# Optimization experiments

Measured on AMD Instinct MI355X. Metric: run time of the kernel, lower is better.

## Reference

```python
import jax, jax.numpy as jnp
import numpy as np

N = 20000      # nodes
E = 160000     # edges (avg degree 16)
IN_DIM = 256
HID = 128      # hidden_dim == per-head out_channels in PyG TransformerConv
HEADS = 4
EPS = 1e-5


def setup_inputs() -> dict:
    key = jax.random.key(0)
    ks = jax.random.split(key, 24)

    def w(k, shape, scale=0.05):
        return jax.random.normal(k, shape, dtype=jnp.float32) * scale

    inp = {
        "x": jax.random.normal(ks[0], (N, IN_DIM), dtype=jnp.float32),
        "edge_index": jax.random.randint(ks[1], (2, E), 0, N, dtype=jnp.int32),
        # input projection
        "lin_w": w(ks[2], (IN_DIM, HID)), "lin_b": jnp.zeros((HID,), jnp.float32),
    }
    i = 3
    for l in (1, 2):
        inp[f"q_w{l}"] = w(ks[i], (HID, HEADS * HID)); i += 1
        inp[f"q_b{l}"] = jnp.zeros((HEADS * HID,), jnp.float32)
        inp[f"k_w{l}"] = w(ks[i], (HID, HEADS * HID)); i += 1
        inp[f"k_b{l}"] = jnp.zeros((HEADS * HID,), jnp.float32)
        inp[f"v_w{l}"] = w(ks[i], (HID, HEADS * HID)); i += 1
        inp[f"v_b{l}"] = jnp.zeros((HEADS * HID,), jnp.float32)
        inp[f"s_w{l}"] = w(ks[i], (HID, HID)); i += 1
        inp[f"s_b{l}"] = jnp.zeros((HID,), jnp.float32)
        inp[f"ln_g{l}"] = jnp.ones((HID,), jnp.float32)
        inp[f"ln_b{l}"] = jnp.zeros((HID,), jnp.float32)
    return inp


def _segment_softmax(scores, seg, num):
    # scores: [E, HEADS], seg: [E] destination indices
    m = jax.ops.segment_max(scores, seg, num_segments=num)
    m = jnp.where(jnp.isfinite(m), m, 0.0)  # guard empty segments
    e = jnp.exp(scores - m[seg])
    d = jax.ops.segment_sum(e, seg, num_segments=num)
    return e / (d[seg] + 1e-16)


def _transformer_conv(x, src, dst, qw, qb, kw, kb, vw, vb, sw, sb):
    # PyG TransformerConv(HID, HID, heads=HEADS, concat=False)
    n = x.shape[0]
    q = (x @ qw + qb).reshape(n, HEADS, HID)
    k = (x @ kw + kb).reshape(n, HEADS, HID)
    v = (x @ vw + vb).reshape(n, HEADS, HID)
    # per-edge attention: query at dst (i), key/value at src (j)
    alpha = jnp.einsum("ehd,ehd->eh", q[dst], k[src]) / jnp.sqrt(jnp.float32(HID))
    alpha = _segment_softmax(alpha, dst, n)                 # [E, HEADS]
    msg = v[src] * alpha[..., None]                          # [E, HEADS, HID]
    out = jax.ops.segment_sum(msg, dst, num_segments=n)      # [N, HEADS, HID]
    out = out.mean(axis=1)                                   # concat=False -> head mean
    return out + x @ sw + sb                                 # root skip connection


def _layer_norm(x, g, b):
    mu = x.mean(-1, keepdims=True)
    var = ((x - mu) ** 2).mean(-1, keepdims=True)
    return (x - mu) * jax.lax.rsqrt(var + EPS) * g + b


def reference(x, edge_index, lin_w, lin_b,
              q_w1, q_b1, k_w1, k_b1, v_w1, v_b1, s_w1, s_b1, ln_g1, ln_b1,
              q_w2, q_b2, k_w2, k_b2, v_w2, v_b2, s_w2, s_b2, ln_g2, ln_b2):
    src, dst = edge_index[0], edge_index[1]
    h = jax.nn.relu(x @ lin_w + lin_b)
    h1 = _transformer_conv(h, src, dst, q_w1, q_b1, k_w1, k_b1, v_w1, v_b1, s_w1, s_b1)
    h = _layer_norm(h1 + h, ln_g1, ln_b1)
    h2 = _transformer_conv(h, src, dst, q_w2, q_b2, k_w2, k_b2, v_w2, v_b2, s_w2, s_b2)
    h = _layer_norm(h2 + h, ln_g2, ln_b2)
    return h
```

## Files before the change

### kernel.cpp

```cpp
#include <hip/hip_runtime.h>
#include <math.h>

#define NNODE 20000
#define NEDGE 160000
#define IN_DIMV 256
#define HIDV 128
#define DEGCAP 64

typedef __attribute__((ext_vector_type(8))) short bf16x8;
typedef __attribute__((ext_vector_type(4))) float f32x4;
typedef __attribute__((ext_vector_type(2))) float f32x2;

__device__ __forceinline__ float bf2f(unsigned short u) {
    union { unsigned int i; float f; } x; x.i = ((unsigned int)u) << 16; return x.f;
}
__device__ __forceinline__ unsigned short f2bf(float f) {
    union { float f; unsigned int i; } x; x.f = f;
    unsigned int r = x.i + 0x7fffu + ((x.i >> 16) & 1u);
    return (unsigned short)(r >> 16);
}
__device__ __forceinline__ void unpack8(uint4 p, float* f) {
    f[0] = bf2f((unsigned short)(p.x & 0xffff)); f[1] = bf2f((unsigned short)(p.x >> 16));
    f[2] = bf2f((unsigned short)(p.y & 0xffff)); f[3] = bf2f((unsigned short)(p.y >> 16));
    f[4] = bf2f((unsigned short)(p.z & 0xffff)); f[5] = bf2f((unsigned short)(p.z >> 16));
    f[6] = bf2f((unsigned short)(p.w & 0xffff)); f[7] = bf2f((unsigned short)(p.w >> 16));
}
__device__ __forceinline__ void unpack8f8_w(unsigned int a, unsigned int b, float* f) {
    f32x2 t;
    t = __builtin_amdgcn_cvt_pk_f32_fp8((int)a, false); f[0] = t.x; f[1] = t.y;
    t = __builtin_amdgcn_cvt_pk_f32_fp8((int)a, true);  f[2] = t.x; f[3] = t.y;
    t = __builtin_amdgcn_cvt_pk_f32_fp8((int)b, false); f[4] = t.x; f[5] = t.y;
    t = __builtin_amdgcn_cvt_pk_f32_fp8((int)b, true);  f[6] = t.x; f[7] = t.y;
}
__device__ __forceinline__ void unpack16f8(uint4 p, float* f) {
    unpack8f8_w(p.x, p.y, f);
    unpack8f8_w(p.z, p.w, f + 8);
}
__device__ __forceinline__ unsigned char f2fp8(float v) {
    int pk = __builtin_amdgcn_cvt_pk_fp8_f32(v, v, 0, false);
    return (unsigned char)(pk & 0xff);
}
__device__ __forceinline__ void gld_lds16(const unsigned short* g, unsigned short* l) {
    __builtin_amdgcn_global_load_lds((const __attribute__((address_space(1))) void*)g,
                                     (__attribute__((address_space(3))) void*)l, 16, 0, 0);
}

__global__ void convert_kernel(
    const float* __restrict__ x, const float* __restrict__ lin_w,
    const float* __restrict__ qw0, const float* __restrict__ kw0,
    const float* __restrict__ vw0, const float* __restrict__ sw0,
    const float* __restrict__ qw1, const float* __restrict__ kw1,
    const float* __restrict__ vw1, const float* __restrict__ sw1,
    unsigned short* __restrict__ xbf, unsigned short* __restrict__ arena)
{
    int idx = blockIdx.x * 256 + threadIdx.x;
    if (idx < 5120000) { xbf[idx] = f2bf(x[idx]); return; }
    int id2 = idx - 5120000;
    if (id2 >= 458752) return;
    float v;
    if (id2 < 32768) {
        int n = id2 >> 8, k = id2 & 255;
        v = lin_w[k * 128 + n];
    } else {
        int t = id2 - 32768;
        int l = t / 212992, r = t % 212992;
        int n = r >> 7, k = r & 127;
        const float* qw = l ? qw1 : qw0;
        const float* kw = l ? kw1 : kw0;
        const float* vw = l ? vw1 : vw0;
        const float* sw = l ? sw1 : sw0;
        if (n < 1536) {
            const float* w = (n < 512) ? qw : (n < 1024) ? kw : vw;
            v = w[k * 512 + (n & 511)];
        } else {
            v = sw[k * 128 + (n - 1536)];
        }
    }
    arena[id2] = f2bf(v);
}

template <int MODE, int K>
__global__ __launch_bounds__(256) void mfma_gemm(
    const unsigned short* __restrict__ A, const unsigned short* __restrict__ WT,
    const float* __restrict__ b0, const float* __restrict__ b1,
    const float* __restrict__ b2, const float* __restrict__ b3,
    unsigned short* __restrict__ qb_out, unsigned char* __restrict__ kv8_out,
    unsigned short* __restrict__ pre16_out, unsigned short* __restrict__ hbf_out)
{
    constexpr bool FULLK = (K == 128);
    __shared__ unsigned short smem[FULLK ? 32768 : 8192];
    unsigned short* ot = smem;
    unsigned char* ot8 = (unsigned char*)smem;

    int tid = threadIdx.x;
    int lane = tid & 63;
    int w = tid >> 6;
    int wm = w & 1, wn = w >> 1;
    int bm = blockIdx.x * 128;
    int bn = blockIdx.y * 128;

    int srow = lane >> 2;
    int scol = (lane & 3) * 8;
    int ar0 = bm + w * 32 + srow;      if (ar0 > NNODE - 1) ar0 = NNODE - 1;
    int ar1 = bm + w * 32 + 16 + srow; if (ar1 > NNODE - 1) ar1 = NNODE - 1;
    int br0 = bn + w * 32 + srow;
    int br1 = bn + w * 32 + 16 + srow;

    f32x4 acc[4][4] = {};
    int arow = wm * 64 + (lane & 15);
    int brow = wn * 64 + (lane & 15);
    int koff = (lane >> 4) * 8;

    if constexpr (FULLK) {
        unsigned short* As = smem;
        unsigned short* Bs = smem + 16384;
#pragma unroll
        for (int c = 0; c < 4; c++) {
            int k0 = c * 32;
            gld_lds16(A + (size_t)ar0 * K + k0 + scol, As + c * 4096 + (w * 32) * 32);
            gld_lds16(A + (size_t)ar1 * K + k0 + scol, As + c * 4096 + (w * 32 + 16) * 32);
            gld_lds16(WT + (size_t)br0 * K + k0 + scol, Bs + c * 4096 + (w * 32) * 32);
            gld_lds16(WT + (size_t)br1 * K + k0 + scol, Bs + c * 4096 + (w * 32 + 16) * 32);
        }
        __syncthreads();
#pragma unroll
        for (int c = 0; c < 4; c++) {
            bf16x8 fa[4], fb[4];
#pragma unroll
            for (int i = 0; i < 4; i++) fa[i] = *(const bf16x8*)&As[c * 4096 + (arow + i * 16) * 32 + koff];
#pragma unroll
            for (int i = 0; i < 4; i++) fb[i] = *(const bf16x8*)&Bs[c * 4096 + (brow + i * 16) * 32 + koff];
#pragma unroll
            for (int mi = 0; mi < 4; mi++)
#pragma unroll
                for (int ni = 0; ni < 4; ni++)
                    acc[mi][ni] = __builtin_amdgcn_mfma_f32_16x16x32_bf16(fa[mi], fb[ni], acc[mi][ni], 0, 0, 0);
        }
    } else {
        unsigned short* As = smem;
        unsigned short* Bs = smem + 4096;
        for (int k0 = 0; k0 < K; k0 += 32) {
            gld_lds16(A + (size_t)ar0 * K + k0 + scol, As + (w * 32) * 32);
            gld_lds16(A + (size_t)ar1 * K + k0 + scol, As + (w * 32 + 16) * 32);
            gld_lds16(WT + (size_t)br0 * K + k0 + scol, Bs + (w * 32) * 32);
            gld_lds16(WT + (size_t)br1 * K + k0 + scol, Bs + (w * 32 + 16) * 32);
            __syncthreads();
            bf16x8 fa[4], fb[4];
#pragma unroll
            for (int i = 0; i < 4; i++) fa[i] = *(const bf16x8*)&As[(arow + i * 16) * 32 + koff];
#pragma unroll
            for (int i = 0; i < 4; i++) fb[i] = *(const bf16x8*)&Bs[(brow + i * 16) * 32 + koff];
#pragma unroll
            for (int mi = 0; mi < 4; mi++)
#pragma unroll
                for (int ni = 0; ni < 4; ni++)
                    acc[mi][ni] = __builtin_amdgcn_mfma_f32_16x16x32_bf16(fa[mi], fb[ni], acc[mi][ni], 0, 0, 0);
            __syncthreads();
        }
    }

    int quad = lane >> 4, lcol = lane & 15;

    if (MODE == 1 && bn >= 512 && bn < 1536) {
        const float* bb = (bn < 1024) ? (b1 + bn - 512) : (b2 + bn - 1024);
        int coff = bn - 512;
#pragma unroll
        for (int hh = 0; hh < 2; hh++) {
            __syncthreads();
            if (wm == hh) {
#pragma unroll
                for (int mi = 0; mi < 4; mi++) {
#pragma unroll
                    for (int ni = 0; ni < 4; ni++) {
                        int lc = wn * 64 + ni * 16 + lcol;
                        float bias = bb[lc];
#pragma unroll
                        for (int reg = 0; reg < 4; reg++) {
                            int lr = mi * 16 + quad * 4 + reg;
                            ot8[lr * 128 + lc] = f2fp8(acc[mi][ni][reg] + bias);
                        }
                    }
                }
            }
            __syncthreads();
            int r = tid >> 2, ch = tid & 3;
            int row = bm + hh * 64 + r;
            if (row < NNODE) {
                uint4* dp = (uint4*)(kv8_out + (size_t)row * 1024 + coff + ch * 32);
                const uint4* sp = (const uint4*)(ot8 + r * 128 + ch * 32);
                dp[0] = sp[0];
                dp[1] = sp[1];
            }
        }
        return;
    }

    unsigned short* dst;
    int dstride, coloff;
    const float* bb;
    if (MODE == 0)           { dst = hbf_out;   dstride = HIDV; coloff = 0;  bb = b0; }
    else if (bn < 512)       { dst = qb_out;    dstride = 512;  coloff = bn; bb = b0 + bn; }
    else                     { dst = pre16_out; dstride = HIDV; coloff = 0;  bb = b3; }

#pragma unroll
    for (int hh = 0; hh < 2; hh++) {
        __syncthreads();
        if (wm == hh) {
#pragma unroll
            for (int mi = 0; mi < 4; mi++) {
#pragma unroll
                for (int ni = 0; ni < 4; ni++) {
                    int lc = wn * 64 + ni * 16 + lcol;
                    float bias = bb[lc];
#pragma unroll
                    for (int reg = 0; reg < 4; reg++) {
                        float v = acc[mi][ni][reg] + bias;
                        if (MODE == 0) v = fmaxf(v, 0.f);
                        ot[(mi * 16 + quad * 4 + reg) * 128 + lc] = f2bf(v);
                    }
                }
            }
        }
        __syncthreads();
        int r = tid >> 2, ch = tid & 3;
        int row = bm + hh * 64 + r;
        if (row < NNODE) {
            uint4* dp = (uint4*)(dst + (size_t)row * dstride + coloff + ch * 32);
            const uint4* sp = (const uint4*)(ot + r * 128 + ch * 32);
#pragma unroll
            for (int q = 0; q < 4; q++) dp[q] = sp[q];
        }
    }
}

__global__ void scatter_kernel(const int* __restrict__ ei, int* __restrict__ cursor,
                               int* __restrict__ bucket) {
    int e = blockIdx.x * blockDim.x + threadIdx.x;
    if (e < NEDGE) {
        int d = ei[NEDGE + e];
        int slot = atomicAdd(&cursor[d], 1);
        if (slot < DEGCAP) bucket[d * DEGCAP + slot] = ei[e];
    }
}

__global__ __launch_bounds__(256) void attn_ln_kernel(
    const unsigned short* __restrict__ qb, const unsigned char* __restrict__ kv8,
    const int* __restrict__ cursor, const int* __restrict__ bucket,
    const unsigned short* __restrict__ pre16, const float* __restrict__ g,
    const float* __restrict__ b,
    unsigned short* __restrict__ hbf ,
    float* __restrict__ extout)
{
    int lane = threadIdx.x & 63;
    int wid = threadIdx.x >> 6;
    int half = lane >> 5;
    int sub = lane & 31;
    int i = blockIdx.x * 8 + wid * 2 + half;
    int cnt = cursor[i]; if (cnt > DEGCAP) cnt = DEGCAP;
    const int* bk = bucket + i * DEGCAP;

    float qr[16];
    {
        const unsigned short* qp = qb + (size_t)i * 512 + sub * 16;
        unpack8(*(const uint4*)qp, qr);
        unpack8(*(const uint4*)(qp + 8), qr + 8);
#pragma unroll
        for (int j = 0; j < 16; j++) qr[j] *= 0.0883883476483184f;
    }

    float m = -INFINITY, l = 0.f;
    float acc[16];
#pragma unroll
    for (int c = 0; c < 16; c++) acc[c] = 0.f;

    if (cnt > 0) {
        int nidx[4];
        uint4 kc[4], vc[4];
#pragma unroll
        for (int t = 0; t < 4; t++) {
            int s = bk[(t < cnt) ? t : (cnt - 1)];
            const unsigned char* r = kv8 + (size_t)s * 1024 + sub * 16;
            kc[t] = *(const uint4*)r;
            vc[t] = *(const uint4*)(r + 512);
            nidx[t] = (4 + t < cnt) ? bk[4 + t] : 0;
        }

        for (int j0 = 0; j0 < cnt; j0 += 4) {
            uint4 kn[4], vn[4];
            bool more = (j0 + 4) < cnt;
            if (more) {
#pragma unroll
                for (int t = 0; t < 4; t++) {
                    const unsigned char* r = kv8 + (size_t)nidx[t] * 1024 + sub * 16;
                    kn[t] = *(const uint4*)r;
                    vn[t] = *(const uint4*)(r + 512);
                    nidx[t] = (j0 + 8 + t < cnt) ? bk[j0 + 8 + t] : 0;
                }
            }
            float d[4];
#pragma unroll
            for (int u = 0; u < 4; u++) {
                float kf[16];
                unpack16f8(kc[u], kf);
                float s0 = 0.f;
#pragma unroll
                for (int c = 0; c < 16; c++) s0 += qr[c] * kf[c];
                d[u] = s0;
            }
#pragma unroll
            for (int u = 0; u < 4; u++) d[u] += __shfl_xor(d[u], 4);
#pragma unroll
            for (int u = 0; u < 4; u++) d[u] += __shfl_xor(d[u], 2);
#pragma unroll
            for (int u = 0; u < 4; u++) d[u] += __shfl_xor(d[u], 1);
#pragma unroll
            for (int u = 0; u < 4; u++) if (j0 + u >= cnt) d[u] = -3.0e38f;
            float mq = fmaxf(fmaxf(d[0], d[1]), fmaxf(d[2], d[3]));
            float mn = fmaxf(m, mq);
            float scale = __expf(m - mn);
            float p0 = __expf(d[0] - mn), p1 = __expf(d[1] - mn);
            float p2 = __expf(d[2] - mn), p3 = __expf(d[3] - mn);
            l = l * scale + ((p0 + p1) + (p2 + p3));
            m = mn;
#pragma unroll
            for (int c = 0; c < 16; c++) acc[c] *= scale;
            float pp[4] = {p0, p1, p2, p3};
#pragma unroll
            for (int u = 0; u < 4; u++) {
                float vf[16];
                unpack16f8(vc[u], vf);
                float pu = pp[u];
#pragma unroll
                for (int c = 0; c < 16; c++) acc[c] += pu * vf[c];
            }
            if (more) {
#pragma unroll
                for (int t = 0; t < 4; t++) { kc[t] = kn[t]; vc[t] = vn[t]; }
            }
        }
    }

    float linv = 0.25f / (l + 1e-16f);
#pragma unroll
    for (int c = 0; c < 16; c++) acc[c] *= linv;
#pragma unroll
    for (int c = 0; c < 16; c++) {
        acc[c] += __shfl_xor(acc[c], 8);
        acc[c] += __shfl_xor(acc[c], 16);
    }

    int cg = sub & 7;
    size_t base = (size_t)i * HIDV + cg * 16;
    float pv[16], hv[16];
    unpack8(((const uint4*)(pre16 + base))[0], pv);
    unpack8(((const uint4*)(pre16 + base))[1], pv + 8);
    unpack8(((const uint4*)(hbf + base))[0], hv);
    unpack8(((const uint4*)(hbf + base))[1], hv + 8);
    float vals[16];
#pragma unroll
    for (int c = 0; c < 16; c++) vals[c] = acc[c] + pv[c] + hv[c];

    float s = 0.f;
#pragma unroll
    for (int c = 0; c < 16; c++) s += vals[c];
    s += __shfl_xor(s, 1); s += __shfl_xor(s, 2); s += __shfl_xor(s, 4);
    float mu = s * (1.f / 128.f);
    float vs = 0.f;
#pragma unroll
    for (int c = 0; c < 16; c++) { float dx = vals[c] - mu; vs += dx * dx; }
    vs += __shfl_xor(vs, 1); vs += __shfl_xor(vs, 2); vs += __shfl_xor(vs, 4);
    float rstd = rsqrtf(vs * (1.f / 128.f) + 1e-5f);

    float gv[16], bv[16];
#pragma unroll
    for (int q = 0; q < 4; q++) {
        float4 gg = ((const float4*)(g + cg * 16))[q];
        float4 bb = ((const float4*)(b + cg * 16))[q];
        gv[q * 4 + 0] = gg.x; gv[q * 4 + 1] = gg.y; gv[q * 4 + 2] = gg.z; gv[q * 4 + 3] = gg.w;
        bv[q * 4 + 0] = bb.x; bv[q * 4 + 1] = bb.y; bv[q * 4 + 2] = bb.z; bv[q * 4 + 3] = bb.w;
    }
    float y[16];
#pragma unroll
    for (int c = 0; c < 16; c++) y[c] = (vals[c] - mu) * rstd * gv[c] + bv[c];

    if (sub < 8) {
        unsigned short tmp[16];
#pragma unroll
        for (int c = 0; c < 16; c++) tmp[c] = f2bf(y[c]);
        ((uint4*)(hbf + base))[0] = ((uint4*)tmp)[0];
        ((uint4*)(hbf + base))[1] = ((uint4*)tmp)[1];
        if (extout) {
#pragma unroll
            for (int q = 0; q < 4; q++)
                ((float4*)(extout + base))[q] = make_float4(y[q * 4 + 0], y[q * 4 + 1], y[q * 4 + 2], y[q * 4 + 3]);
        }
    }
}

extern "C" void kernel_launch(void* const* d_in, const int* in_sizes, int n_in,
                              void* d_out, int out_size, void* d_ws, size_t ws_size,
                              hipStream_t stream) {
    const float* x = (const float*)d_in[0];
    const int* ei = (const int*)d_in[1];

    char* ws = (char*)d_ws;
    unsigned short* hbf = (unsigned short*)(ws + 0);
    unsigned short* pre16 = (unsigned short*)(ws + 5120000);
    unsigned short* qb = (unsigned short*)(ws + 10240000);
    unsigned char* kv8 = (unsigned char*)(ws + 30720000);
    unsigned short* xbf = (unsigned short*)(ws + 51200000);
    int* cursor = (int*)(ws + 61440000);
    int* bucket = (int*)(ws + 61520000);
    unsigned short* arena = (unsigned short*)(ws + 66640000);

    convert_kernel<<<21793, 256, 0, stream>>>(
        x, (const float*)d_in[2],
        (const float*)d_in[4], (const float*)d_in[6], (const float*)d_in[8], (const float*)d_in[10],
        (const float*)d_in[14], (const float*)d_in[16], (const float*)d_in[18], (const float*)d_in[20],
        xbf, arena);

    hipMemsetAsync(cursor, 0, NNODE * sizeof(int), stream);
    scatter_kernel<<<(NEDGE + 255) / 256, 256, 0, stream>>>(ei, cursor, bucket);

    const int GM = (NNODE + 127) / 128;

    mfma_gemm<0, 256><<<dim3(GM, 1), 256, 0, stream>>>(
        xbf, arena, (const float*)d_in[3], nullptr, nullptr, nullptr,
        nullptr, nullptr, nullptr, hbf);

    for (int l = 0; l < 2; l++) {
        int o = 4 + l * 10;
        const unsigned short* WT = arena + 32768 + l * 212992;
        mfma_gemm<1, 128><<<dim3(GM, 13), 256, 0, stream>>>(
            hbf, WT,
            (const float*)d_in[o + 1], (const float*)d_in[o + 3],
            (const float*)d_in[o + 5], (const float*)d_in[o + 7],
            qb, kv8, pre16, nullptr);

        attn_ln_kernel<<<NNODE / 8, 256, 0, stream>>>(
            qb, kv8, cursor, bucket, pre16,
            (const float*)d_in[o + 8], (const float*)d_in[o + 9],
            hbf, (l == 1) ? (float*)d_out : nullptr);
    }
}
```

Baseline: 296.8 us.

## Stage neighbor K/V rows into per-wave LDS ring via global_load_lds

Result: no change. 299.0 us (+0.7%).

```diff
diff --git a/kernel.cpp b/kernel.cpp
--- a/kernel.cpp
+++ b/kernel.cpp
@@ -6,6 +6,7 @@
 #define IN_DIMV 256
 #define HIDV 128
 #define DEGCAP 64
+#define RING 8
 
 typedef __attribute__((ext_vector_type(8))) short bf16x8;
 typedef __attribute__((ext_vector_type(4))) float f32x4;
@@ -32,15 +33,15 @@
     t = __builtin_amdgcn_cvt_pk_f32_fp8((int)b, false); f[4] = t.x; f[5] = t.y;
     t = __builtin_amdgcn_cvt_pk_f32_fp8((int)b, true);  f[6] = t.x; f[7] = t.y;
 }
-__device__ __forceinline__ void unpack16f8(uint4 p, float* f) {
-    unpack8f8_w(p.x, p.y, f);
-    unpack8f8_w(p.z, p.w, f + 8);
-}
 __device__ __forceinline__ unsigned char f2fp8(float v) {
     int pk = __builtin_amdgcn_cvt_pk_fp8_f32(v, v, 0, false);
     return (unsigned char)(pk & 0xff);
 }
 __device__ __forceinline__ void gld_lds16(const unsigned short* g, unsigned short* l) {
+    __builtin_amdgcn_global_load_lds((const __attribute__((address_space(1))) void*)g,
+                                     (__attribute__((address_space(3))) void*)l, 16, 0, 0);
+}
+__device__ __forceinline__ void gld_lds16b(const unsigned char* g, unsigned char* l) {
     __builtin_amdgcn_global_load_lds((const __attribute__((address_space(1))) void*)g,
                                      (__attribute__((address_space(3))) void*)l, 16, 0, 0);
 }
@@ -251,148 +252,134 @@
     unsigned short* __restrict__ hbf ,
     float* __restrict__ extout)
 {
+    __shared__ __align__(16) unsigned char ring[4][RING * 1024];
     int lane = threadIdx.x & 63;
     int wid = threadIdx.x >> 6;
-    int half = lane >> 5;
-    int sub = lane & 31;
-    int i = blockIdx.x * 8 + wid * 2 + half;
+    int i = blockIdx.x * 4 + wid;
     int cnt = cursor[i]; if (cnt > DEGCAP) cnt = DEGCAP;
     const int* bk = bucket + i * DEGCAP;
-
-    float qr[16];
+    unsigned char* myring = ring[wid];
+
+    int hg = lane >> 4;
+    int sl = lane & 15;
+
+    float qr[8];
     {
-        const unsigned short* qp = qb + (size_t)i * 512 + sub * 16;
-        unpack8(*(const uint4*)qp, qr);
-        unpack8(*(const uint4*)(qp + 8), qr + 8);
-#pragma unroll
-        for (int j = 0; j < 16; j++) qr[j] *= 0.0883883476483184f;
+        uint4 p = *(const uint4*)(qb + (size_t)i * 512 + lane * 8);
+        unpack8(p, qr);
+#pragma unroll
+        for (int j = 0; j < 8; j++) qr[j] *= 0.0883883476483184f;
     }
 
     float m = -INFINITY, l = 0.f;
-    float acc[16];
-#pragma unroll
-    for (int c = 0; c < 16; c++) acc[c] = 0.f;
-
-    if (cnt > 0) {
-        int nidx[4];
-        uint4 kc[4], vc[4];
-#pragma unroll
-        for (int t = 0; t < 4; t++) {
-            int s = bk[(t < cnt) ? t : (cnt - 1)];
-            const unsigned char* r = kv8 + (size_t)s * 1024 + sub * 16;
-            kc[t] = *(const uint4*)r;
-            vc[t] = *(const uint4*)(r + 512);
-            nidx[t] = (4 + t < cnt) ? bk[4 + t] : 0;
-        }
-
-        for (int j0 = 0; j0 < cnt; j0 += 4) {
-            uint4 kn[4], vn[4];
-            bool more = (j0 + 4) < cnt;
-            if (more) {
-#pragma unroll
-                for (int t = 0; t < 4; t++) {
-                    const unsigned char* r = kv8 + (size_t)nidx[t] * 1024 + sub * 16;
-                    kn[t] = *(const uint4*)r;
-                    vn[t] = *(const uint4*)(r + 512);
-                    nidx[t] = (j0 + 8 + t < cnt) ? bk[j0 + 8 + t] : 0;
-                }
-            }
-            float d[4];
-#pragma unroll
-            for (int u = 0; u < 4; u++) {
-                float kf[16];
-                unpack16f8(kc[u], kf);
-                float s0 = 0.f;
-#pragma unroll
-                for (int c = 0; c < 16; c++) s0 += qr[c] * kf[c];
-                d[u] = s0;
-            }
-#pragma unroll
-            for (int u = 0; u < 4; u++) d[u] += __shfl_xor(d[u], 4);
-#pragma unroll
-            for (int u = 0; u < 4; u++) d[u] += __shfl_xor(d[u], 2);
-#pragma unroll
-            for (int u = 0; u < 4; u++) d[u] += __shfl_xor(d[u], 1);
-#pragma unroll
-            for (int u = 0; u < 4; u++) if (j0 + u >= cnt) d[u] = -3.0e38f;
-            float mq = fmaxf(fmaxf(d[0], d[1]), fmaxf(d[2], d[3]));
-            float mn = fmaxf(m, mq);
-            float scale = __expf(m - mn);
-            float p0 = __expf(d[0] - mn), p1 = __expf(d[1] - mn);
-            float p2 = __expf(d[2] - mn), p3 = __expf(d[3] - mn);
-            l = l * scale + ((p0 + p1) + (p2 + p3));
-            m = mn;
-#pragma unroll
-            for (int c = 0; c < 16; c++) acc[c] *= scale;
-            float pp[4] = {p0, p1, p2, p3};
-#pragma unroll
-            for (int u = 0; u < 4; u++) {
-                float vf[16];
-                unpack16f8(vc[u], vf);
-                float pu = pp[u];
-#pragma unroll
-                for (int c = 0; c < 16; c++) acc[c] += pu * vf[c];
-            }
-            if (more) {
-#pragma unroll
-                for (int t = 0; t < 4; t++) { kc[t] = kn[t]; vc[t] = vn[t]; }
-            }
+    float acc[8] = {0.f, 0.f, 0.f, 0.f, 0.f, 0.f, 0.f, 0.f};
+
+    for (int j0 = 0; j0 < cnt; j0 += RING) {
+        int nb = cnt - j0; if (nb > RING) nb = RING;
+        int myidx = bk[j0 + ((lane < nb) ? lane : 0)];
+        asm volatile("s_waitcnt lgkmcnt(0)" ::: "memory");
+#pragma unroll
+        for (int t = 0; t < RING; t++) {
+            if (t >= nb) break;
+            int src = __shfl(myidx, t);
+            gld_lds16b(kv8 + (size_t)src * 1024 + lane * 16, myring + t * 1024);
+        }
+        asm volatile("s_waitcnt vmcnt(0)" ::: "memory");
+
+        float d[RING];
+#pragma unroll
+        for (int t = 0; t < RING; t++) d[t] = -3.0e38f;
+#pragma unroll
+        for (int t = 0; t < RING; t++) {
+            if (t >= nb) break;
+            uint2 kk = *(const uint2*)(myring + t * 1024 + hg * 128 + sl * 8);
+            float kf[8];
+            unpack8f8_w(kk.x, kk.y, kf);
+            float s0 = qr[0] * kf[0] + qr[1] * kf[1] + qr[2] * kf[2] + qr[3] * kf[3] +
+                       qr[4] * kf[4] + qr[5] * kf[5] + qr[6] * kf[6] + qr[7] * kf[7];
+            d[t] = s0;
+        }
+#pragma unroll
+        for (int t = 0; t < RING; t++) { if (t >= nb) break; d[t] += __shfl_xor(d[t], 8); }
+#pragma unroll
+        for (int t = 0; t < RING; t++) { if (t >= nb) break; d[t] += __shfl_xor(d[t], 4); }
+#pragma unroll
+        for (int t = 0; t < RING; t++) { if (t >= nb) break; d[t] += __shfl_xor(d[t], 2); }
+#pragma unroll
+        for (int t = 0; t < RING; t++) { if (t >= nb) break; d[t] += __shfl_xor(d[t], 1); }
+
+        float mq = d[0];
+#pragma unroll
+        for (int t = 1; t < RING; t++) mq = fmaxf(mq, d[t]);
+        float mn = fmaxf(m, mq);
+        float scale = __expf(m - mn);
+        float p[RING];
+        float psum = 0.f;
+#pragma unroll
+        for (int t = 0; t < RING; t++) { p[t] = __expf(d[t] - mn); psum += p[t]; }
+        l = l * scale + psum;
+        m = mn;
+#pragma unroll
+        for (int c = 0; c < 8; c++) acc[c] *= scale;
+#pragma unroll
+        for (int t = 0; t < RING; t++) {
+            if (t >= nb) break;
+            uint2 vv = *(const uint2*)(myring + t * 1024 + 512 + hg * 128 + sl * 8);
+            float vf[8];
+            unpack8f8_w(vv.x, vv.y, vf);
+            float pt = p[t];
+#pragma unroll
+            for (int c = 0; c < 8; c++) acc[c] += pt * vf[c];
         }
     }
 
     float linv = 0.25f / (l + 1e-16f);
 #pragma unroll
-    for (int c = 0; c < 16; c++) acc[c] *= linv;
-#pragma unroll
-    for (int c = 0; c < 16; c++) {
-        acc[c] += __shfl_xor(acc[c], 8);
+    for (int c = 0; c < 8; c++) acc[c] *= linv;
+#pragma unroll
+    for (int c = 0; c < 8; c++) {
         acc[c] += __shfl_xor(acc[c], 16);
-    }
-
-    int cg = sub & 7;
-    size_t base = (size_t)i * HIDV + cg * 16;
-    float pv[16], hv[16];
-    unpack8(((const uint4*)(pre16 + base))[0], pv);
-    unpack8(((const uint4*)(pre16 + base))[1], pv + 8);
-    unpack8(((const uint4*)(hbf + base))[0], hv);
-    unpack8(((const uint4*)(hbf + base))[1], hv + 8);
-    float vals[16];
-#pragma unroll
-    for (int c = 0; c < 16; c++) vals[c] = acc[c] + pv[c] + hv[c];
+        acc[c] += __shfl_xor(acc[c], 32);
+    }
+
+    size_t base = (size_t)i * HIDV + sl * 8;
+    float pv[8], hv[8];
+    unpack8(*(const uint4*)(pre16 + base), pv);
+    unpack8(*(const uint4*)(hbf + base), hv);
+    float vals[8];
+#pragma unroll
+    for (int c = 0; c < 8; c++) vals[c] = acc[c] + pv[c] + hv[c];
 
     float s = 0.f;
 #pragma unroll
-    for (int c = 0; c < 16; c++) s += vals[c];
-    s += __shfl_xor(s, 1); s += __shfl_xor(s, 2); s += __shfl_xor(s, 4);
+    for (int c = 0; c < 8; c++) s += vals[c];
+    s += __shfl_xor(s, 1); s += __shfl_xor(s, 2);
+    s += __shfl_xor(s, 4); s += __shfl_xor(s, 8);
     float mu = s * (1.f / 128.f);
     float vs = 0.f;
 #pragma unroll
-    for (int c = 0; c < 16; c++) { float dx = vals[c] - mu; vs += dx * dx; }
-    vs += __shfl_xor(vs, 1); vs += __shfl_xor(vs, 2); vs += __shfl_xor(vs, 4);
+    for (int c = 0; c < 8; c++) { float dx = vals[c] - mu; vs += dx * dx; }
+    vs += __shfl_xor(vs, 1); vs += __shfl_xor(vs, 2);
+    vs += __shfl_xor(vs, 4); vs += __shfl_xor(vs, 8);
     float rstd = rsqrtf(vs * (1.f / 128.f) + 1e-5f);
 
-    float gv[16], bv[16];
-#pragma unroll
-    for (int q = 0; q < 4; q++) {
-        float4 gg = ((const float4*)(g + cg * 16))[q];
-        float4 bb = ((const float4*)(b + cg * 16))[q];
-        gv[q * 4 + 0] = gg.x; gv[q * 4 + 1] = gg.y; gv[q * 4 + 2] = gg.z; gv[q * 4 + 3] = gg.w;
-        bv[q * 4 + 0] = bb.x; bv[q * 4 + 1] = bb.y; bv[q * 4 + 2] = bb.z; bv[q * 4 + 3] = bb.w;
-    }
-    float y[16];
-#pragma unroll
-    for (int c = 0; c < 16; c++) y[c] = (vals[c] - mu) * rstd * gv[c] + bv[c];
-
-    if (sub < 8) {
-        unsigned short tmp[16];
-#pragma unroll
-        for (int c = 0; c < 16; c++) tmp[c] = f2bf(y[c]);
-        ((uint4*)(hbf + base))[0] = ((uint4*)tmp)[0];
-        ((uint4*)(hbf + base))[1] = ((uint4*)tmp)[1];
+    float4 g0 = ((const float4*)(g + sl * 8))[0];
+    float4 g1 = ((const float4*)(g + sl * 8))[1];
+    float4 bb0 = ((const float4*)(b + sl * 8))[0];
+    float4 bb1 = ((const float4*)(b + sl * 8))[1];
+    float y[8];
+    y[0] = (vals[0] - mu) * rstd * g0.x + bb0.x; y[1] = (vals[1] - mu) * rstd * g0.y + bb0.y;
+    y[2] = (vals[2] - mu) * rstd * g0.z + bb0.z; y[3] = (vals[3] - mu) * rstd * g0.w + bb0.w;
+    y[4] = (vals[4] - mu) * rstd * g1.x + bb1.x; y[5] = (vals[5] - mu) * rstd * g1.y + bb1.y;
+    y[6] = (vals[6] - mu) * rstd * g1.z + bb1.z; y[7] = (vals[7] - mu) * rstd * g1.w + bb1.w;
+
+    if (lane < 16) {
+        unsigned short tmp[8] = {f2bf(y[0]), f2bf(y[1]), f2bf(y[2]), f2bf(y[3]),
+                                 f2bf(y[4]), f2bf(y[5]), f2bf(y[6]), f2bf(y[7])};
+        *(uint4*)(hbf + base) = *(uint4*)tmp;
         if (extout) {
-#pragma unroll
-            for (int q = 0; q < 4; q++)
-                ((float4*)(extout + base))[q] = make_float4(y[q * 4 + 0], y[q * 4 + 1], y[q * 4 + 2], y[q * 4 + 3]);
+            ((float4*)(extout + base))[0] = make_float4(y[0], y[1], y[2], y[3]);
+            ((float4*)(extout + base))[1] = make_float4(y[4], y[5], y[6], y[7]);
         }
     }
 }
@@ -437,7 +424,7 @@
             (const float*)d_in[o + 5], (const float*)d_in[o + 7],
             qb, kv8, pre16, nullptr);
 
-        attn_ln_kernel<<<NNODE / 8, 256, 0, stream>>>(
+        attn_ln_kernel<<<NNODE / 4, 256, 0, stream>>>(
             qb, kv8, cursor, bucket, pre16,
             (const float*)d_in[o + 8], (const float*)d_in[o + 9],
             hbf, (l == 1) ? (float*)d_out : nullptr);
```
